# Kernel tuning notes

Measured on AMD Instinct MI355X. Metric: run time of the kernel, lower is better.

## Reference

```python
import jax, jax.numpy as jnp
import numpy as np

DIM = 1024
DEPTH = 8
HEADS = 16
DIM_HEAD = 64
INNER = HEADS * DIM_HEAD  # 1024
NQ = 64
EMB = 768
OUT = 1024
FF_INNER = 4 * DIM
B, N1 = 32, 257
EPS = 1e-5


def layer_norm(x, g, b):
    m = jnp.mean(x, axis=-1, keepdims=True)
    v = jnp.mean(jnp.square(x - m), axis=-1, keepdims=True)
    return (x - m) * jax.lax.rsqrt(v + EPS) * g + b


def split_heads(t):
    # (b, l, inner) -> (b, h, l, dh)
    b, l, _ = t.shape
    return t.reshape(b, l, HEADS, DIM_HEAD).transpose(0, 2, 1, 3)


def setup_inputs() -> dict:
    key = jax.random.key(0)
    ks = jax.random.split(key, 12)
    s = 0.02
    inp = {
        "x": jax.random.normal(ks[0], (B, N1, EMB), jnp.float32),
        "latents": jax.random.normal(ks[1], (1, NQ, DIM), jnp.float32) / np.sqrt(DIM),
        "proj_in_w": jax.random.normal(ks[2], (EMB, DIM), jnp.float32) * s,
        "proj_in_b": jnp.zeros((DIM,), jnp.float32),
        "ln1_g": jnp.ones((DEPTH, DIM), jnp.float32),
        "ln1_b": jnp.zeros((DEPTH, DIM), jnp.float32),
        "ln2_g": jnp.ones((DEPTH, DIM), jnp.float32),
        "ln2_b": jnp.zeros((DEPTH, DIM), jnp.float32),
        "Wq": jax.random.normal(ks[3], (DEPTH, DIM, INNER), jnp.float32) * s,
        "Wkv": jax.random.normal(ks[4], (DEPTH, DIM, 2 * INNER), jnp.float32) * s,
        "Wo": jax.random.normal(ks[5], (DEPTH, INNER, DIM), jnp.float32) * s,
        "ff_ln_g": jnp.ones((DEPTH, DIM), jnp.float32),
        "ff_ln_b": jnp.zeros((DEPTH, DIM), jnp.float32),
        "ff_w1": jax.random.normal(ks[6], (DEPTH, DIM, FF_INNER), jnp.float32) * s,
        "ff_w2": jax.random.normal(ks[7], (DEPTH, FF_INNER, DIM), jnp.float32) * s,
        "proj_out_w": jax.random.uniform(ks[8], (DIM, OUT), jnp.float32, -0.01, 0.01),
        "proj_out_b": jnp.zeros((OUT,), jnp.float32),
        "norm_out_g": jnp.ones((OUT,), jnp.float32),
        "norm_out_b": jnp.zeros((OUT,), jnp.float32),
    }
    return inp


def reference(x, latents, proj_in_w, proj_in_b, ln1_g, ln1_b, ln2_g, ln2_b,
              Wq, Wkv, Wo, ff_ln_g, ff_ln_b, ff_w1, ff_w2,
              proj_out_w, proj_out_b, norm_out_g, norm_out_b):
    # proj_in
    xf = x @ proj_in_w + proj_in_b              # (b, n1, dim)
    lat = jnp.broadcast_to(latents, (x.shape[0], NQ, DIM))
    scale = DIM_HEAD ** -0.25                   # 1/sqrt(sqrt(dim_head))

    for i in range(DEPTH):
        # PerceiverAttention
        xn = layer_norm(xf, ln1_g[i], ln1_b[i])
        ln_lat = layer_norm(lat, ln2_g[i], ln2_b[i])
        q = split_heads(ln_lat @ Wq[i])                       # (b,h,nq,dh)
        kv = jnp.concatenate([xn, ln_lat], axis=1) @ Wkv[i]   # (b,n1+nq,2*inner)
        k, v = jnp.split(kv, 2, axis=-1)
        k, v = split_heads(k), split_heads(v)                 # (b,h,nk,dh)
        w = jnp.einsum('bhqd,bhkd->bhqk', q * scale, k * scale)
        w = jax.nn.softmax(w.astype(jnp.float32), axis=-1).astype(q.dtype)
        o = jnp.einsum('bhqk,bhkd->bhqd', w, v)               # (b,h,nq,dh)
        o = o.transpose(0, 2, 1, 3).reshape(lat.shape[0], NQ, INNER)
        lat = o @ Wo[i] + lat
        # FeedForward: LN -> Linear -> GELU -> Linear
        h = layer_norm(lat, ff_ln_g[i], ff_ln_b[i])
        h = jax.nn.gelu(h @ ff_w1[i], approximate=False) @ ff_w2[i]
        lat = h + lat

    out = lat @ proj_out_w + proj_out_b
    return layer_norm(out, norm_out_g, norm_out_b)
```

## Files before the change

kernel.cpp:

```cpp
#include <hip/hip_runtime.h>
#include <hip/hip_bf16.h>
#include <cstdint>

typedef __hip_bfloat16 bf16;
typedef __attribute__((ext_vector_type(8))) short short8;
typedef __attribute__((ext_vector_type(4))) float f32x4;

__device__ __forceinline__ f32x4 mfma16(short8 a, short8 b, f32x4 c) {
  return __builtin_amdgcn_mfma_f32_16x16x32_bf16(a, b, c, 0, 0, 0);
}

__device__ __forceinline__ void gload16(const bf16* g, bf16* l) {
  __builtin_amdgcn_global_load_lds((const __attribute__((address_space(1))) void*)g,
                                   (__attribute__((address_space(3))) void*)l, 16, 0, 0);
}


__global__ void __launch_bounds__(256) cvt_f32_bf16(const float* __restrict__ in,
                                                    bf16* __restrict__ out, int n) {
  int i = blockIdx.x * 256 + threadIdx.x;
  if (i < n) out[i] = __float2bfloat16(in[i]);
}

__global__ void __launch_bounds__(256) bcast_latents(const float* __restrict__ lin,
                                                     float* __restrict__ lat) {
  int i = blockIdx.x * 256 + threadIdx.x;
  lat[i] = lin[i & 65535];
}


__device__ __forceinline__ void trans_tile(float (*tile)[33], const float* __restrict__ src,
                                           bf16* __restrict__ dst, int K, int N,
                                           int bx, int by) {
  int n0 = bx * 32, k0 = by * 32;
  int tx = threadIdx.x & 31, ty = threadIdx.x >> 5;
#pragma unroll
  for (int j = 0; j < 32; j += 8)
    tile[ty + j][tx] = src[(size_t)(k0 + ty + j) * N + n0 + tx];
  __syncthreads();
#pragma unroll
  for (int j = 0; j < 32; j += 8)
    dst[(size_t)(n0 + ty + j) * K + k0 + tx] = __float2bfloat16(tile[tx][ty + j]);
}

__global__ void __launch_bounds__(256) transpose_cvt(const float* __restrict__ src,
                                                     bf16* __restrict__ dst,
                                                     int K, int N) {
  __shared__ float tile[32][33];
  trans_tile(tile, src, dst, K, N, blockIdx.x, blockIdx.y);
}

__global__ void __launch_bounds__(256) transpose_all(
    const float* __restrict__ wq, const float* __restrict__ wkv,
    const float* __restrict__ wo, const float* __restrict__ w1,
    const float* __restrict__ w2, bf16* __restrict__ wq_t, bf16* __restrict__ wkv_t,
    bf16* __restrict__ wo_t, bf16* __restrict__ w1_t, bf16* __restrict__ w2_t) {
  __shared__ float tile[32][33];
  int id = blockIdx.x;
  if (id < 1024) {
    trans_tile(tile, wq, wq_t, 1024, 1024, id & 31, id >> 5);
  } else if (id < 3072) {
    id -= 1024;
    trans_tile(tile, wkv, wkv_t, 1024, 2048, id & 63, id >> 6);
  } else if (id < 4096) {
    id -= 3072;
    trans_tile(tile, wo, wo_t, 1024, 1024, id & 31, id >> 5);
  } else if (id < 8192) {
    id -= 4096;
    trans_tile(tile, w1, w1_t, 1024, 4096, id & 127, id >> 7);
  } else {
    id -= 8192;
    trans_tile(tile, w2, w2_t, 4096, 1024, id & 31, id >> 5);
  }
}


__device__ __forceinline__ void row_stats(const float* x, int tid, float v[4],
                                          float& mean, float& rstd, float* red) {
  float s = 0.f, s2 = 0.f;
#pragma unroll
  for (int j = 0; j < 4; j++) {
    v[j] = x[tid + j * 256];
    s += v[j]; s2 += v[j] * v[j];
  }
#pragma unroll
  for (int o = 32; o > 0; o >>= 1) {
    s += __shfl_down(s, o);
    s2 += __shfl_down(s2, o);
  }
  int w = tid >> 6;
  if ((tid & 63) == 0) { red[w] = s; red[4 + w] = s2; }
  __syncthreads();
  s = red[0] + red[1] + red[2] + red[3];
  s2 = red[4] + red[5] + red[6] + red[7];
  mean = s * (1.f / 1024.f);
  float var = s2 * (1.f / 1024.f) - mean * mean;
  rstd = rsqrtf(var + 1e-5f);
}

__global__ void __launch_bounds__(256) ln_to_bf16(const float* __restrict__ in,
                                                  const float* __restrict__ g,
                                                  const float* __restrict__ bb,
                                                  bf16* __restrict__ out) {
  __shared__ float red[8];
  int row = blockIdx.x, tid = threadIdx.x;
  const float* x = in + (size_t)row * 1024;
  float v[4], mean, rstd;
  row_stats(x, tid, v, mean, rstd, red);
  bf16* o1 = out + (size_t)row * 1024;
#pragma unroll
  for (int j = 0; j < 4; j++) {
    int c = tid + j * 256;
    float y = (v[j] - mean) * rstd;
    if (g) y = y * g[c] + bb[c];
    o1[c] = __float2bfloat16(y);
  }
}

__global__ void __launch_bounds__(256) ln_to_f32(const float* __restrict__ in,
                                                 const float* __restrict__ g,
                                                 const float* __restrict__ bb,
                                                 float* __restrict__ out) {
  __shared__ float red[8];
  int row = blockIdx.x, tid = threadIdx.x;
  const float* x = in + (size_t)row * 1024;
  float v[4], mean, rstd;
  row_stats(x, tid, v, mean, rstd, red);
  float* o1 = out + (size_t)row * 1024;
#pragma unroll
  for (int j = 0; j < 4; j++) {
    int c = tid + j * 256;
    o1[c] = (v[j] - mean) * rstd * g[c] + bb[c];
  }
}

__global__ void __launch_bounds__(256) lncat(const bf16* __restrict__ xhat,
                                             const float* __restrict__ lat,
                                             const float* __restrict__ g1,
                                             const float* __restrict__ b1,
                                             const float* __restrict__ g2,
                                             const float* __restrict__ b2,
                                             bf16* __restrict__ cat,
                                             bf16* __restrict__ lnlat) {
  __shared__ float red[8];
  int row = blockIdx.x, tid = threadIdx.x;
  int bidx = row / 336, n = row - bidx * 336;
  bf16* out = cat + (size_t)row * 1024;
  if (n < 257) {
    const bf16* in = xhat + ((size_t)bidx * 257 + n) * 1024;
#pragma unroll
    for (int j = 0; j < 4; j++) {
      int c = tid + j * 256;
      out[c] = __float2bfloat16(__bfloat162float(in[c]) * g1[c] + b1[c]);
    }
  } else if (n < 321) {
    int lrow = bidx * 64 + (n - 257);
    const float* x = lat + (size_t)lrow * 1024;
    float v[4], mean, rstd;
    row_stats(x, tid, v, mean, rstd, red);
    bf16* o2 = lnlat + (size_t)lrow * 1024;
#pragma unroll
    for (int j = 0; j < 4; j++) {
      int c = tid + j * 256;
      bf16 hh = __float2bfloat16((v[j] - mean) * rstd * g2[c] + b2[c]);
      out[c] = hh;
      o2[c] = hh;
    }
  } else {
#pragma unroll
    for (int j = 0; j < 4; j++)
      out[tid + j * 256] = __float2bfloat16(0.f);
  }
}


enum { MB_BIAS = 1, MB_RESID = 2, MB_GELU = 4, MB_BF16 = 8 };

template <int MODE>
__global__ void __launch_bounds__(256, 2) gemm_bt(
    const bf16* __restrict__ A, const bf16* __restrict__ Bt,
    void* __restrict__ Cout, const float* __restrict__ bias,
    const float* __restrict__ resid, int M, int N, int K) {
  __shared__ bf16 sA[128 * 32];
  __shared__ bf16 sB[128 * 32];
  int tid = threadIdx.x;
  int wave = tid >> 6, lane = tid & 63;
  int quad = lane >> 4, l16 = lane & 15;
  int wm = (wave >> 1) * 64, wn = (wave & 1) * 64;
  int m0 = blockIdx.y * 128, n0 = blockIdx.x * 128;
  int z = blockIdx.z;
  int kPer = K / gridDim.z;
  int kBeg = z * kPer, kEnd = kBeg + kPer;

  int srow = wave * 16 + (lane >> 2);
  int scol = (lane & 3) * 8;
  const bf16* gA0 = A + (size_t)min(m0 + srow, M - 1) * K + scol;
  const bf16* gA1 = A + (size_t)min(m0 + 64 + srow, M - 1) * K + scol;
  const bf16* gB0 = Bt + (size_t)(n0 + srow) * K + scol;
  const bf16* gB1 = Bt + (size_t)(n0 + 64 + srow) * K + scol;
  bf16* lA0 = &sA[(wave * 16) * 32];
  bf16* lA1 = &sA[(64 + wave * 16) * 32];
  bf16* lB0 = &sB[(wave * 16) * 32];
  bf16* lB1 = &sB[(64 + wave * 16) * 32];

  f32x4 acc[4][4] = {};

  for (int k0 = kBeg; k0 < kEnd; k0 += 32) {
    gload16(gA0 + k0, lA0);
    gload16(gA1 + k0, lA1);
    gload16(gB0 + k0, lB0);
    gload16(gB1 + k0, lB1);
    __syncthreads();
    short8 af[4], bfv[4];
#pragma unroll
    for (int i = 0; i < 4; i++)
      af[i] = *(const short8*)&sA[(wm + i * 16 + l16) * 32 + quad * 8];
#pragma unroll
    for (int j = 0; j < 4; j++)
      bfv[j] = *(const short8*)&sB[(wn + j * 16 + l16) * 32 + quad * 8];
#pragma unroll
    for (int i = 0; i < 4; i++)
#pragma unroll
      for (int j = 0; j < 4; j++)
        acc[i][j] = mfma16(af[i], bfv[j], acc[i][j]);
    __syncthreads();
  }

  float* cf = (float*)Cout + (size_t)z * ((size_t)M * N);
#pragma unroll
  for (int i = 0; i < 4; i++) {
    int grb = m0 + wm + i * 16 + quad * 4;
#pragma unroll
    for (int j = 0; j < 4; j++) {
      int gc = n0 + wn + j * 16 + l16;
      float bv = (MODE & MB_BIAS) ? bias[gc] : 0.f;
#pragma unroll
      for (int r = 0; r < 4; r++) {
        int gr = grb + r;
        if (gr < M) {
          float vv = acc[i][j][r] + bv;
          if (MODE & MB_GELU) vv = 0.5f * vv * (1.f + erff(vv * 0.70710678118654752f));
          if (MODE & MB_RESID) vv += resid[(size_t)gr * N + gc];
          if (MODE & MB_BF16) ((bf16*)Cout)[(size_t)gr * N + gc] = __float2bfloat16(vv);
          else cf[(size_t)gr * N + gc] = vv;
        }
      }
    }
  }
}


enum { RD_BIAS = 1, RD_RESID = 2, RD_BF16 = 4 };

template <int MODE>
__global__ void __launch_bounds__(256) reduce_k(const float* __restrict__ parts, int S,
                                                int MN, int N,
                                                const float* __restrict__ bias,
                                                const float* __restrict__ resid,
                                                void* __restrict__ out) {
  int i4 = (blockIdx.x * 256 + threadIdx.x) * 4;
  if (i4 >= MN) return;
  float4 a = *(const float4*)&parts[i4];
#pragma unroll 4
  for (int s = 1; s < S; s++) {
    float4 b = *(const float4*)&parts[(size_t)s * MN + i4];
    a.x += b.x; a.y += b.y; a.z += b.z; a.w += b.w;
  }
  if (MODE & RD_BIAS) {
    float4 b = *(const float4*)&bias[i4 & (N - 1)];
    a.x += b.x; a.y += b.y; a.z += b.z; a.w += b.w;
  }
  if (MODE & RD_RESID) {
    float4 b = *(const float4*)&resid[i4];
    a.x += b.x; a.y += b.y; a.z += b.z; a.w += b.w;
  }
  if (MODE & RD_BF16) {
    bf16 o[4] = {__float2bfloat16(a.x), __float2bfloat16(a.y),
                 __float2bfloat16(a.z), __float2bfloat16(a.w)};
    *(uint2*)&((bf16*)out)[i4] = *(uint2*)o;
  } else {
    *(float4*)&((float*)out)[i4] = a;
  }
}


__global__ void __launch_bounds__(256, 2) attn(const bf16* __restrict__ qb,
                                               const bf16* __restrict__ kvb,
                                               bf16* __restrict__ ob) {
  __shared__ bf16 sQ[64 * 64];
  __shared__ bf16 sKV[64 * 64];
  __shared__ bf16 sP[64 * 368];
  __shared__ float sRed[256];

  int h = blockIdx.x, b = blockIdx.y;
  int tid = threadIdx.x, wave = tid >> 6, lane = tid & 63;
  int quad = lane >> 4, l16 = lane & 15;

  const bf16* qg = qb + (size_t)b * 64 * 1024 + h * 64;
  const bf16* kg = kvb + (size_t)b * 336 * 2048 + h * 64;
  const bf16* vg = kg + 1024;

  {
    int r = tid >> 3, c = (tid & 7) * 8;
    *(uint4*)&sQ[r * 64 + c] = *(const uint4*)&qg[(size_t)r * 1024 + c];
    *(uint4*)&sQ[(r + 32) * 64 + c] = *(const uint4*)&qg[(size_t)(r + 32) * 1024 + c];
  }

  f32x4 accS[6][4] = {};

  for (int g = 0; g < 6; g++) {
    __syncthreads();
    {
      int r = tid >> 3, c = (tid & 7) * 8;
      int gr = g * 64 + r;
      if (gr < 336) *(uint4*)&sKV[r * 64 + c] = *(const uint4*)&kg[(size_t)gr * 2048 + c];
      gr += 32;
      if (gr < 336) *(uint4*)&sKV[(r + 32) * 64 + c] = *(const uint4*)&kg[(size_t)gr * 2048 + c];
    }
    __syncthreads();
    if (g * 4 + wave < 21) {
#pragma unroll
      for (int ks = 0; ks < 2; ks++) {
        short8 bfr = *(const short8*)&sKV[(wave * 16 + l16) * 64 + ks * 32 + quad * 8];
#pragma unroll
        for (int i = 0; i < 4; i++) {
          short8 afr = *(const short8*)&sQ[(i * 16 + l16) * 64 + ks * 32 + quad * 8];
          accS[g][i] = mfma16(afr, bfr, accS[g][i]);
        }
      }
    }
  }

  float rmax[4][4], rsum[4][4];
#pragma unroll
  for (int i = 0; i < 4; i++)
#pragma unroll
    for (int r = 0; r < 4; r++) { rmax[i][r] = -1e30f; rsum[i][r] = 0.f; }

#pragma unroll
  for (int g = 0; g < 6; g++) {
    int col = (g * 4 + wave) * 16 + l16;
    bool valid = col < 321;
#pragma unroll
    for (int i = 0; i < 4; i++)
#pragma unroll
      for (int r = 0; r < 4; r++) {
        float v = accS[g][i][r] * 0.125f;
        accS[g][i][r] = v;
        if (valid) rmax[i][r] = fmaxf(rmax[i][r], v);
      }
  }
#pragma unroll
  for (int off = 1; off < 16; off <<= 1)
#pragma unroll
    for (int i = 0; i < 4; i++)
#pragma unroll
      for (int r = 0; r < 4; r++)
        rmax[i][r] = fmaxf(rmax[i][r], __shfl_xor(rmax[i][r], off));
  if (l16 == 0) {
#pragma unroll
    for (int i = 0; i < 4; i++)
#pragma unroll
      for (int r = 0; r < 4; r++)
        sRed[wave * 64 + i * 16 + quad * 4 + r] = rmax[i][r];
  }
  __syncthreads();
#pragma unroll
  for (int i = 0; i < 4; i++)
#pragma unroll
    for (int r = 0; r < 4; r++) {
      int row = i * 16 + quad * 4 + r;
      rmax[i][r] = fmaxf(fmaxf(sRed[row], sRed[64 + row]),
                         fmaxf(sRed[128 + row], sRed[192 + row]));
    }
  __syncthreads();

#pragma unroll
  for (int g = 0; g < 6; g++) {
    int col = (g * 4 + wave) * 16 + l16;
    bool valid = col < 321;
#pragma unroll
    for (int i = 0; i < 4; i++)
#pragma unroll
      for (int r = 0; r < 4; r++) {
        float pv = valid ? __expf(accS[g][i][r] - rmax[i][r]) : 0.f;
        rsum[i][r] += pv;
        if (col < 352) sP[(i * 16 + quad * 4 + r) * 368 + col] = __float2bfloat16(pv);
      }
  }
#pragma unroll
  for (int off = 1; off < 16; off <<= 1)
#pragma unroll
    for (int i = 0; i < 4; i++)
#pragma unroll
      for (int r = 0; r < 4; r++)
        rsum[i][r] += __shfl_xor(rsum[i][r], off);
  if (l16 == 0) {
#pragma unroll
    for (int i = 0; i < 4; i++)
#pragma unroll
      for (int r = 0; r < 4; r++)
        sRed[wave * 64 + i * 16 + quad * 4 + r] = rsum[i][r];
  }
  __syncthreads();
#pragma unroll
  for (int i = 0; i < 4; i++)
#pragma unroll
    for (int r = 0; r < 4; r++) {
      int row = i * 16 + quad * 4 + r;
      rsum[i][r] = sRed[row] + sRed[64 + row] + sRed[128 + row] + sRed[192 + row];
    }

  f32x4 accO[4] = {};
  const short* sKVs = (const short*)sKV;
  for (int cch = 0; cch < 6; cch++) {
    __syncthreads();
    {
      int r = tid >> 3, c = (tid & 7) * 8;
      int gr = cch * 64 + r;
      if (gr < 336) *(uint4*)&sKV[r * 64 + c] = *(const uint4*)&vg[(size_t)gr * 2048 + c];
      gr += 32;
      if (gr < 336) *(uint4*)&sKV[(r + 32) * 64 + c] = *(const uint4*)&vg[(size_t)gr * 2048 + c];
    }
    __syncthreads();
    int nks = (cch == 5) ? 1 : 2;
    for (int ks = 0; ks < nks; ks++) {
      short8 bv;
#pragma unroll
      for (int jj = 0; jj < 8; jj++)
        bv[jj] = sKVs[(ks * 32 + quad * 8 + jj) * 64 + wave * 16 + l16];
#pragma unroll
      for (int i = 0; i < 4; i++) {
        short8 ap = *(const short8*)&sP[(i * 16 + l16) * 368 + cch * 64 + ks * 32 + quad * 8];
        accO[i] = mfma16(ap, bv, accO[i]);
      }
    }
  }

#pragma unroll
  for (int i = 0; i < 4; i++)
#pragma unroll
    for (int r = 0; r < 4; r++) {
      int row = i * 16 + quad * 4 + r;
      ob[(size_t)(b * 64 + row) * 1024 + h * 64 + wave * 16 + l16] =
          __float2bfloat16(accO[i][r] / rsum[i][r]);
    }
}


extern "C" void kernel_launch(void* const* d_in, const int* in_sizes, int n_in,
                              void* d_out, int out_size, void* d_ws, size_t ws_size,
                              hipStream_t stream) {
  (void)in_sizes; (void)n_in; (void)out_size; (void)ws_size;
  const float* x    = (const float*)d_in[0];
  const float* lin  = (const float*)d_in[1];
  const float* piw  = (const float*)d_in[2];
  const float* pib  = (const float*)d_in[3];
  const float* ln1g = (const float*)d_in[4];
  const float* ln1b = (const float*)d_in[5];
  const float* ln2g = (const float*)d_in[6];
  const float* ln2b = (const float*)d_in[7];
  const float* Wq   = (const float*)d_in[8];
  const float* Wkv  = (const float*)d_in[9];
  const float* Wo   = (const float*)d_in[10];
  const float* ffg  = (const float*)d_in[11];
  const float* ffb  = (const float*)d_in[12];
  const float* W1   = (const float*)d_in[13];
  const float* W2   = (const float*)d_in[14];
  const float* poW  = (const float*)d_in[15];
  const float* pob  = (const float*)d_in[16];
  const float* nog  = (const float*)d_in[17];
  const float* nob  = (const float*)d_in[18];

  char* p = (char*)d_ws;
  auto alloc = [&](size_t bytes) -> char* {
    char* q = p; p += (bytes + 255) & ~(size_t)255; return q;
  };
  bf16* pin_t  = (bf16*)alloc((size_t)1024 * 768 * 2);
  bf16* pout_t = (bf16*)alloc((size_t)1024 * 1024 * 2);
  bf16* wq_t   = (bf16*)alloc((size_t)1024 * 1024 * 2);
  bf16* wkv_t  = (bf16*)alloc((size_t)2048 * 1024 * 2);
  bf16* wo_t   = (bf16*)alloc((size_t)1024 * 1024 * 2);
  bf16* w1_t   = (bf16*)alloc((size_t)4096 * 1024 * 2);
  bf16* w2_t   = (bf16*)alloc((size_t)1024 * 4096 * 2);
  bf16* x_bf   = (bf16*)alloc((size_t)8224 * 768 * 2);
  float* xf    = (float*)alloc((size_t)8224 * 1024 * 4);
  bf16* xhat   = (bf16*)alloc((size_t)8224 * 1024 * 2);
  bf16* cat    = (bf16*)alloc((size_t)10752 * 1024 * 2);
  bf16* lnlat  = (bf16*)alloc((size_t)2048 * 1024 * 2);
  bf16* qbuf   = (bf16*)alloc((size_t)2048 * 1024 * 2);
  bf16* kvbuf  = (bf16*)alloc((size_t)10752 * 2048 * 2);
  bf16* obuf   = (bf16*)alloc((size_t)2048 * 1024 * 2);
  float* lat   = (float*)alloc((size_t)2048 * 1024 * 4);
  float* lat2  = (float*)alloc((size_t)2048 * 1024 * 4);
  bf16* lnff   = (bf16*)alloc((size_t)2048 * 1024 * 2);
  bf16* h1     = (bf16*)alloc((size_t)2048 * 4096 * 2);
  float* otmp  = (float*)alloc((size_t)2048 * 1024 * 4);

  const int MN = 2048 * 1024;

  cvt_f32_bf16<<<6316032 / 256, 256, 0, stream>>>(x, x_bf, 6316032);
  transpose_cvt<<<dim3(32, 24), 256, 0, stream>>>(piw, pin_t, 768, 1024);
  transpose_cvt<<<dim3(32, 32), 256, 0, stream>>>(poW, pout_t, 1024, 1024);
  bcast_latents<<<8192, 256, 0, stream>>>(lin, lat);
  gemm_bt<MB_BIAS><<<dim3(8, 65), 256, 0, stream>>>(x_bf, pin_t, xf, pib, nullptr,
                                                    8224, 1024, 768);
  ln_to_bf16<<<8224, 256, 0, stream>>>(xf, nullptr, nullptr, xhat);

  for (int i = 0; i < 8; i++) {
    transpose_all<<<12288, 256, 0, stream>>>(
        Wq + (size_t)i * 1048576, Wkv + (size_t)i * 2097152, Wo + (size_t)i * 1048576,
        W1 + (size_t)i * 4194304, W2 + (size_t)i * 4194304,
        wq_t, wkv_t, wo_t, w1_t, w2_t);
    lncat<<<10752, 256, 0, stream>>>(xhat, lat, ln1g + i * 1024, ln1b + i * 1024,
                                     ln2g + i * 1024, ln2b + i * 1024, cat, lnlat);
    gemm_bt<0><<<dim3(8, 16, 4), 256, 0, stream>>>(lnlat, wq_t, xf, nullptr, nullptr,
                                                   2048, 1024, 1024);
    reduce_k<RD_BF16><<<MN / 1024, 256, 0, stream>>>(xf, 4, MN, 1024, nullptr, nullptr, qbuf);
    gemm_bt<MB_BF16><<<dim3(16, 84), 256, 0, stream>>>(cat, wkv_t, kvbuf, nullptr, nullptr,
                                                       10752, 2048, 1024);
    attn<<<dim3(16, 32), 256, 0, stream>>>(qbuf, kvbuf, obuf);
    gemm_bt<0><<<dim3(8, 16, 4), 256, 0, stream>>>(obuf, wo_t, xf, nullptr, nullptr,
                                                   2048, 1024, 1024);
    reduce_k<RD_RESID><<<MN / 1024, 256, 0, stream>>>(xf, 4, MN, 1024, nullptr, lat, lat2);
    ln_to_bf16<<<2048, 256, 0, stream>>>(lat2, ffg + i * 1024, ffb + i * 1024, lnff);
    gemm_bt<MB_GELU | MB_BF16><<<dim3(32, 16), 256, 0, stream>>>(lnff, w1_t, h1, nullptr,
                                                                 nullptr, 2048, 4096, 1024);
    gemm_bt<0><<<dim3(8, 16, 4), 256, 0, stream>>>(h1, w2_t, xf, nullptr, nullptr,
                                                   2048, 1024, 4096);
    reduce_k<RD_RESID><<<MN / 1024, 256, 0, stream>>>(xf, 4, MN, 1024, nullptr, lat2, lat);
  }

  cvt_f32_bf16<<<2097152 / 256, 256, 0, stream>>>(lat, lnff, 2097152);
  gemm_bt<0><<<dim3(8, 16, 4), 256, 0, stream>>>(lnff, pout_t, xf, nullptr, nullptr,
                                                 2048, 1024, 1024);
  reduce_k<RD_BIAS><<<MN / 1024, 256, 0, stream>>>(xf, 4, MN, 1024, pob, nullptr, otmp);
  ln_to_f32<<<2048, 256, 0, stream>>>(otmp, nog, nob, (float*)d_out);
}
```

Measured before the change: 2.189 ms.

## Fuse split-K reductions with layernorms, merge Q and KV GEMMs, swizzle attention LDS

Split-K partial-sum reductions are folded into the following layernorm kernels: the attention residual goes into the FF layernorm, the FF residual into the next layer's lncat, and the output bias into the final layernorm. This removes separate launches and several round trips through global memory. The Q projection now runs without split-K inside one launch with the KV GEMM, so its reduce kernel also goes away. The attention kernel uses an XOR-swizzled LDS layout for Q/K/V and pads the P buffer to cut bank conflicts. The price is more kernel variants and a final reduce that has to combine the residual and the bf16 conversion correctly.

```diff
diff --git a/kernel.cpp b/kernel.cpp
--- a/kernel.cpp
+++ b/kernel.cpp
@@ -20,12 +20,6 @@
                                                     bf16* __restrict__ out, int n) {
   int i = blockIdx.x * 256 + threadIdx.x;
   if (i < n) out[i] = __float2bfloat16(in[i]);
-}
-
-__global__ void __launch_bounds__(256) bcast_latents(const float* __restrict__ lin,
-                                                     float* __restrict__ lat) {
-  int i = blockIdx.x * 256 + threadIdx.x;
-  lat[i] = lin[i & 65535];
 }
 
 
@@ -75,14 +69,11 @@
 }
 
 
-__device__ __forceinline__ void row_stats(const float* x, int tid, float v[4],
-                                          float& mean, float& rstd, float* red) {
+__device__ __forceinline__ void stats_of(const float v[4], int tid, float& mean,
+                                         float& rstd, float* red) {
   float s = 0.f, s2 = 0.f;
 #pragma unroll
-  for (int j = 0; j < 4; j++) {
-    v[j] = x[tid + j * 256];
-    s += v[j]; s2 += v[j] * v[j];
-  }
+  for (int j = 0; j < 4; j++) { s += v[j]; s2 += v[j] * v[j]; }
 #pragma unroll
   for (int o = 32; o > 0; o >>= 1) {
     s += __shfl_down(s, o);
@@ -96,6 +87,13 @@
   mean = s * (1.f / 1024.f);
   float var = s2 * (1.f / 1024.f) - mean * mean;
   rstd = rsqrtf(var + 1e-5f);
+}
+
+__device__ __forceinline__ void row_stats(const float* x, int tid, float v[4],
+                                          float& mean, float& rstd, float* red) {
+#pragma unroll
+  for (int j = 0; j < 4; j++) v[j] = x[tid + j * 256];
+  stats_of(v, tid, mean, rstd, red);
 }
 
 __global__ void __launch_bounds__(256) ln_to_bf16(const float* __restrict__ in,
@@ -117,25 +115,12 @@
   }
 }
 
-__global__ void __launch_bounds__(256) ln_to_f32(const float* __restrict__ in,
-                                                 const float* __restrict__ g,
-                                                 const float* __restrict__ bb,
-                                                 float* __restrict__ out) {
-  __shared__ float red[8];
-  int row = blockIdx.x, tid = threadIdx.x;
-  const float* x = in + (size_t)row * 1024;
-  float v[4], mean, rstd;
-  row_stats(x, tid, v, mean, rstd, red);
-  float* o1 = out + (size_t)row * 1024;
-#pragma unroll
-  for (int j = 0; j < 4; j++) {
-    int c = tid + j * 256;
-    o1[c] = (v[j] - mean) * rstd * g[c] + bb[c];
-  }
-}
-
+template <int LM>
 __global__ void __launch_bounds__(256) lncat(const bf16* __restrict__ xhat,
-                                             const float* __restrict__ lat,
+                                             const float* __restrict__ lin,
+                                             const float* __restrict__ parts,
+                                             const float* __restrict__ lat2,
+                                             float* __restrict__ lat,
                                              const float* __restrict__ g1,
                                              const float* __restrict__ b1,
                                              const float* __restrict__ g2,
@@ -146,6 +131,7 @@
   int row = blockIdx.x, tid = threadIdx.x;
   int bidx = row / 336, n = row - bidx * 336;
   bf16* out = cat + (size_t)row * 1024;
+  const size_t MN = (size_t)2048 * 1024;
   if (n < 257) {
     const bf16* in = xhat + ((size_t)bidx * 257 + n) * 1024;
 #pragma unroll
@@ -155,9 +141,23 @@
     }
   } else if (n < 321) {
     int lrow = bidx * 64 + (n - 257);
-    const float* x = lat + (size_t)lrow * 1024;
-    float v[4], mean, rstd;
-    row_stats(x, tid, v, mean, rstd, red);
+    float v[4];
+#pragma unroll
+    for (int j = 0; j < 4; j++) {
+      int c = tid + j * 256;
+      size_t idx = (size_t)lrow * 1024 + c;
+      float a;
+      if (LM == 0) {
+        a = lin[(size_t)(n - 257) * 1024 + c];
+      } else {
+        a = parts[idx] + parts[MN + idx] + parts[2 * MN + idx] + parts[3 * MN + idx]
+          + lat2[idx];
+      }
+      lat[idx] = a;
+      v[j] = a;
+    }
+    float mean, rstd;
+    stats_of(v, tid, mean, rstd, red);
     bf16* o2 = lnlat + (size_t)lrow * 1024;
 #pragma unroll
     for (int j = 0; j < 4; j++) {
@@ -177,20 +177,15 @@
 enum { MB_BIAS = 1, MB_RESID = 2, MB_GELU = 4, MB_BF16 = 8 };
 
 template <int MODE>
-__global__ void __launch_bounds__(256, 2) gemm_bt(
-    const bf16* __restrict__ A, const bf16* __restrict__ Bt,
-    void* __restrict__ Cout, const float* __restrict__ bias,
-    const float* __restrict__ resid, int M, int N, int K) {
-  __shared__ bf16 sA[128 * 32];
-  __shared__ bf16 sB[128 * 32];
+__device__ __forceinline__ void gemm_tile(
+    const bf16* __restrict__ A, const bf16* __restrict__ Bt, void* __restrict__ Cout,
+    const float* __restrict__ bias, const float* __restrict__ resid,
+    int M, int N, int K, int m0, int n0, int kBeg, int kEnd, size_t planeOff,
+    bf16* sA, bf16* sB) {
   int tid = threadIdx.x;
   int wave = tid >> 6, lane = tid & 63;
   int quad = lane >> 4, l16 = lane & 15;
   int wm = (wave >> 1) * 64, wn = (wave & 1) * 64;
-  int m0 = blockIdx.y * 128, n0 = blockIdx.x * 128;
-  int z = blockIdx.z;
-  int kPer = K / gridDim.z;
-  int kBeg = z * kPer, kEnd = kBeg + kPer;
 
   int srow = wave * 16 + (lane >> 2);
   int scol = (lane & 3) * 8;
@@ -226,7 +221,7 @@
     __syncthreads();
   }
 
-  float* cf = (float*)Cout + (size_t)z * ((size_t)M * N);
+  float* cf = (float*)Cout + planeOff;
 #pragma unroll
   for (int i = 0; i < 4; i++) {
     int grb = m0 + wm + i * 16 + quad * 4;
@@ -246,6 +241,37 @@
         }
       }
     }
+  }
+}
+
+template <int MODE>
+__global__ void __launch_bounds__(256, 2) gemm_bt(
+    const bf16* __restrict__ A, const bf16* __restrict__ Bt,
+    void* __restrict__ Cout, const float* __restrict__ bias,
+    const float* __restrict__ resid, int M, int N, int K) {
+  __shared__ bf16 sA[128 * 32];
+  __shared__ bf16 sB[128 * 32];
+  int kPer = K / gridDim.z;
+  gemm_tile<MODE>(A, Bt, Cout, bias, resid, M, N, K,
+                  blockIdx.y * 128, blockIdx.x * 128,
+                  blockIdx.z * kPer, (blockIdx.z + 1) * kPer,
+                  (size_t)blockIdx.z * ((size_t)M * N), sA, sB);
+}
+
+__global__ void __launch_bounds__(256, 2) gemm_qkv(
+    const bf16* __restrict__ catb, const bf16* __restrict__ wkv,
+    bf16* __restrict__ kvbuf, const bf16* __restrict__ lnlat,
+    const bf16* __restrict__ wq, bf16* __restrict__ qbuf) {
+  __shared__ bf16 sA[128 * 32];
+  __shared__ bf16 sB[128 * 32];
+  int by = blockIdx.y, bx = blockIdx.x;
+  if (by < 84) {
+    gemm_tile<MB_BF16>(catb, wkv, kvbuf, nullptr, nullptr, 10752, 2048, 1024,
+                       by * 128, bx * 128, 0, 1024, 0, sA, sB);
+  } else {
+    int t = (by - 84) * 16 + bx;
+    gemm_tile<MB_BF16>(lnlat, wq, qbuf, nullptr, nullptr, 2048, 1024, 1024,
+                       (t >> 3) * 128, (t & 7) * 128, 0, 1024, 0, sA, sB);
   }
 }
 
@@ -283,14 +309,72 @@
   }
 }
 
+__global__ void __launch_bounds__(256) reduce_ln_resid(
+    const float* __restrict__ parts, const float* __restrict__ resid,
+    const float* __restrict__ g, const float* __restrict__ bb,
+    float* __restrict__ lat2, bf16* __restrict__ lnff) {
+  __shared__ float red[8];
+  int row = blockIdx.x, tid = threadIdx.x;
+  const size_t MN = (size_t)2048 * 1024;
+  float v[4];
+#pragma unroll
+  for (int j = 0; j < 4; j++) {
+    int c = tid + j * 256;
+    size_t idx = (size_t)row * 1024 + c;
+    float a = parts[idx] + parts[MN + idx] + parts[2 * MN + idx] + parts[3 * MN + idx]
+            + resid[idx];
+    lat2[idx] = a;
+    v[j] = a;
+  }
+  float mean, rstd;
+  stats_of(v, tid, mean, rstd, red);
+  bf16* o = lnff + (size_t)row * 1024;
+#pragma unroll
+  for (int j = 0; j < 4; j++) {
+    int c = tid + j * 256;
+    o[c] = __float2bfloat16((v[j] - mean) * rstd * g[c] + bb[c]);
+  }
+}
+
+__global__ void __launch_bounds__(256) reduce_bias_ln(
+    const float* __restrict__ parts, const float* __restrict__ bias,
+    const float* __restrict__ g, const float* __restrict__ bb,
+    float* __restrict__ out) {
+  __shared__ float red[8];
+  int row = blockIdx.x, tid = threadIdx.x;
+  const size_t MN = (size_t)2048 * 1024;
+  float v[4];
+#pragma unroll
+  for (int j = 0; j < 4; j++) {
+    int c = tid + j * 256;
+    size_t idx = (size_t)row * 1024 + c;
+    v[j] = parts[idx] + parts[MN + idx] + parts[2 * MN + idx] + parts[3 * MN + idx]
+         + bias[c];
+  }
+  float mean, rstd;
+  stats_of(v, tid, mean, rstd, red);
+  float* o = out + (size_t)row * 1024;
+#pragma unroll
+  for (int j = 0; j < 4; j++) {
+    int c = tid + j * 256;
+    o[c] = (v[j] - mean) * rstd * g[c] + bb[c];
+  }
+}
+
+
+__device__ __forceinline__ int swz64(int row, int cb) {
+  return (row << 7) + (cb ^ ((row & 7) << 4) ^ (((row >> 3) & 3) << 5));
+}
 
 __global__ void __launch_bounds__(256, 2) attn(const bf16* __restrict__ qb,
                                                const bf16* __restrict__ kvb,
                                                bf16* __restrict__ ob) {
   __shared__ bf16 sQ[64 * 64];
   __shared__ bf16 sKV[64 * 64];
-  __shared__ bf16 sP[64 * 368];
+  __shared__ bf16 sP[64 * 376];
   __shared__ float sRed[256];
+  char* cQ = (char*)sQ;
+  char* cKV = (char*)sKV;
 
   int h = blockIdx.x, b = blockIdx.y;
   int tid = threadIdx.x, wave = tid >> 6, lane = tid & 63;
@@ -301,9 +385,11 @@
   const bf16* vg = kg + 1024;
 
   {
-    int r = tid >> 3, c = (tid & 7) * 8;
-    *(uint4*)&sQ[r * 64 + c] = *(const uint4*)&qg[(size_t)r * 1024 + c];
-    *(uint4*)&sQ[(r + 32) * 64 + c] = *(const uint4*)&qg[(size_t)(r + 32) * 1024 + c];
+    int r = tid >> 3, cb = (tid & 7) * 16;
+    *(uint4*)(cQ + swz64(r, cb)) =
+        *(const uint4*)((const char*)qg + (size_t)r * 2048 + cb);
+    *(uint4*)(cQ + swz64(r + 32, cb)) =
+        *(const uint4*)((const char*)qg + (size_t)(r + 32) * 2048 + cb);
   }
 
   f32x4 accS[6][4] = {};
@@ -311,20 +397,24 @@
   for (int g = 0; g < 6; g++) {
     __syncthreads();
     {
-      int r = tid >> 3, c = (tid & 7) * 8;
+      int r = tid >> 3, cb = (tid & 7) * 16;
       int gr = g * 64 + r;
-      if (gr < 336) *(uint4*)&sKV[r * 64 + c] = *(const uint4*)&kg[(size_t)gr * 2048 + c];
+      if (gr < 336)
+        *(uint4*)(cKV + swz64(r, cb)) =
+            *(const uint4*)((const char*)kg + (size_t)gr * 4096 + cb);
       gr += 32;
-      if (gr < 336) *(uint4*)&sKV[(r + 32) * 64 + c] = *(const uint4*)&kg[(size_t)gr * 2048 + c];
+      if (gr < 336)
+        *(uint4*)(cKV + swz64(r + 32, cb)) =
+            *(const uint4*)((const char*)kg + (size_t)gr * 4096 + cb);
     }
     __syncthreads();
     if (g * 4 + wave < 21) {
 #pragma unroll
       for (int ks = 0; ks < 2; ks++) {
-        short8 bfr = *(const short8*)&sKV[(wave * 16 + l16) * 64 + ks * 32 + quad * 8];
+        short8 bfr = *(const short8*)(cKV + swz64(wave * 16 + l16, ks * 64 + quad * 16));
 #pragma unroll
         for (int i = 0; i < 4; i++) {
-          short8 afr = *(const short8*)&sQ[(i * 16 + l16) * 64 + ks * 32 + quad * 8];
+          short8 afr = *(const short8*)(cQ + swz64(i * 16 + l16, ks * 64 + quad * 16));
           accS[g][i] = mfma16(afr, bfr, accS[g][i]);
         }
       }
@@ -385,7 +475,7 @@
       for (int r = 0; r < 4; r++) {
         float pv = valid ? __expf(accS[g][i][r] - rmax[i][r]) : 0.f;
         rsum[i][r] += pv;
-        if (col < 352) sP[(i * 16 + quad * 4 + r) * 368 + col] = __float2bfloat16(pv);
+        if (col < 352) sP[(i * 16 + quad * 4 + r) * 376 + col] = __float2bfloat16(pv);
       }
   }
 #pragma unroll
@@ -412,26 +502,30 @@
     }
 
   f32x4 accO[4] = {};
-  const short* sKVs = (const short*)sKV;
   for (int cch = 0; cch < 6; cch++) {
     __syncthreads();
     {
-      int r = tid >> 3, c = (tid & 7) * 8;
+      int r = tid >> 3, cb = (tid & 7) * 16;
       int gr = cch * 64 + r;
-      if (gr < 336) *(uint4*)&sKV[r * 64 + c] = *(const uint4*)&vg[(size_t)gr * 2048 + c];
+      if (gr < 336)
+        *(uint4*)(cKV + swz64(r, cb)) =
+            *(const uint4*)((const char*)vg + (size_t)gr * 4096 + cb);
       gr += 32;
-      if (gr < 336) *(uint4*)&sKV[(r + 32) * 64 + c] = *(const uint4*)&vg[(size_t)gr * 2048 + c];
+      if (gr < 336)
+        *(uint4*)(cKV + swz64(r + 32, cb)) =
+            *(const uint4*)((const char*)vg + (size_t)gr * 4096 + cb);
     }
     __syncthreads();
     int nks = (cch == 5) ? 1 : 2;
     for (int ks = 0; ks < nks; ks++) {
       short8 bv;
+      int cb = (wave * 16 + l16) * 2;
 #pragma unroll
       for (int jj = 0; jj < 8; jj++)
-        bv[jj] = sKVs[(ks * 32 + quad * 8 + jj) * 64 + wave * 16 + l16];
+        bv[jj] = *(const short*)(cKV + swz64(ks * 32 + quad * 8 + jj, cb));
 #pragma unroll
       for (int i = 0; i < 4; i++) {
-        short8 ap = *(const short8*)&sP[(i * 16 + l16) * 368 + cch * 64 + ks * 32 + quad * 8];
+        short8 ap = *(const short8*)&sP[(i * 16 + l16) * 376 + cch * 64 + ks * 32 + quad * 8];
         accO[i] = mfma16(ap, bv, accO[i]);
       }
     }
@@ -495,14 +589,12 @@
   float* lat2  = (float*)alloc((size_t)2048 * 1024 * 4);
   bf16* lnff   = (bf16*)alloc((size_t)2048 * 1024 * 2);
   bf16* h1     = (bf16*)alloc((size_t)2048 * 4096 * 2);
-  float* otmp  = (float*)alloc((size_t)2048 * 1024 * 4);
 
   const int MN = 2048 * 1024;
 
   cvt_f32_bf16<<<6316032 / 256, 256, 0, stream>>>(x, x_bf, 6316032);
   transpose_cvt<<<dim3(32, 24), 256, 0, stream>>>(piw, pin_t, 768, 1024);
   transpose_cvt<<<dim3(32, 32), 256, 0, stream>>>(poW, pout_t, 1024, 1024);
-  bcast_latents<<<8192, 256, 0, stream>>>(lin, lat);
   gemm_bt<MB_BIAS><<<dim3(8, 65), 256, 0, stream>>>(x_bf, pin_t, xf, pib, nullptr,
                                                     8224, 1024, 768);
   ln_to_bf16<<<8224, 256, 0, stream>>>(xf, nullptr, nullptr, xhat);
@@ -512,28 +604,30 @@
         Wq + (size_t)i * 1048576, Wkv + (size_t)i * 2097152, Wo + (size_t)i * 1048576,
         W1 + (size_t)i * 4194304, W2 + (size_t)i * 4194304,
         wq_t, wkv_t, wo_t, w1_t, w2_t);
-    lncat<<<10752, 256, 0, stream>>>(xhat, lat, ln1g + i * 1024, ln1b + i * 1024,
-                                     ln2g + i * 1024, ln2b + i * 1024, cat, lnlat);
-    gemm_bt<0><<<dim3(8, 16, 4), 256, 0, stream>>>(lnlat, wq_t, xf, nullptr, nullptr,
-                                                   2048, 1024, 1024);
-    reduce_k<RD_BF16><<<MN / 1024, 256, 0, stream>>>(xf, 4, MN, 1024, nullptr, nullptr, qbuf);
-    gemm_bt<MB_BF16><<<dim3(16, 84), 256, 0, stream>>>(cat, wkv_t, kvbuf, nullptr, nullptr,
-                                                       10752, 2048, 1024);
+    if (i == 0)
+      lncat<0><<<10752, 256, 0, stream>>>(xhat, lin, nullptr, nullptr, lat,
+                                          ln1g + i * 1024, ln1b + i * 1024,
+                                          ln2g + i * 1024, ln2b + i * 1024, cat, lnlat);
+    else
+      lncat<1><<<10752, 256, 0, stream>>>(xhat, nullptr, xf, lat2, lat,
+                                          ln1g + i * 1024, ln1b + i * 1024,
+                                          ln2g + i * 1024, ln2b + i * 1024, cat, lnlat);
+    gemm_qkv<<<dim3(16, 92), 256, 0, stream>>>(cat, wkv_t, kvbuf, lnlat, wq_t, qbuf);
     attn<<<dim3(16, 32), 256, 0, stream>>>(qbuf, kvbuf, obuf);
     gemm_bt<0><<<dim3(8, 16, 4), 256, 0, stream>>>(obuf, wo_t, xf, nullptr, nullptr,
                                                    2048, 1024, 1024);
-    reduce_k<RD_RESID><<<MN / 1024, 256, 0, stream>>>(xf, 4, MN, 1024, nullptr, lat, lat2);
-    ln_to_bf16<<<2048, 256, 0, stream>>>(lat2, ffg + i * 1024, ffb + i * 1024, lnff);
+    reduce_ln_resid<<<2048, 256, 0, stream>>>(xf, lat, ffg + i * 1024, ffb + i * 1024,
+                                              lat2, lnff);
     gemm_bt<MB_GELU | MB_BF16><<<dim3(32, 16), 256, 0, stream>>>(lnff, w1_t, h1, nullptr,
                                                                  nullptr, 2048, 4096, 1024);
     gemm_bt<0><<<dim3(8, 16, 4), 256, 0, stream>>>(h1, w2_t, xf, nullptr, nullptr,
                                                    2048, 1024, 4096);
-    reduce_k<RD_RESID><<<MN / 1024, 256, 0, stream>>>(xf, 4, MN, 1024, nullptr, lat2, lat);
-  }
-
-  cvt_f32_bf16<<<2097152 / 256, 256, 0, stream>>>(lat, lnff, 2097152);
+    if (i == 7)
+      reduce_k<RD_RESID | RD_BF16><<<MN / 1024, 256, 0, stream>>>(
+          xf, 4, MN, 1024, nullptr, lat2, lnff);
+  }
+
   gemm_bt<0><<<dim3(8, 16, 4), 256, 0, stream>>>(lnff, pout_t, xf, nullptr, nullptr,
                                                  2048, 1024, 1024);
-  reduce_k<RD_BIAS><<<MN / 1024, 256, 0, stream>>>(xf, 4, MN, 1024, pob, nullptr, otmp);
-  ln_to_f32<<<2048, 256, 0, stream>>>(otmp, nog, nob, (float*)d_out);
-}
+  reduce_bias_ln<<<2048, 256, 0, stream>>>(xf, pob, nog, nob, (float*)d_out);
+}
```

After: 2.000 ms. 8.6% less time.
